# Kernel tuning notes

Measured on AMD Instinct MI355X. Metric: run time of the kernel, lower is better.

The kernel has to match this reference:

```python
import jax, jax.numpy as jnp
import numpy as np

DIM = 256
NUM_HEADS = 8


def setup_inputs() -> dict:
    key = jax.random.key(0)
    ks = jax.random.split(key, 8)
    B, H, W = 2, 64, 64
    s = 0.02
    return {
        "query": jax.random.normal(ks[0], (B, H, W, DIM), jnp.float32),
        "sim": jax.random.normal(ks[1], (B, H, W, DIM), jnp.float32),
        "Wq": jax.random.normal(ks[2], (DIM, DIM), jnp.float32) * s,
        "bq": jnp.zeros((DIM,), jnp.float32),
        "Wkv": jax.random.normal(ks[3], (DIM, 2 * DIM), jnp.float32) * s,
        "bkv": jnp.zeros((2 * DIM,), jnp.float32),
        "Wp": jax.random.normal(ks[4], (DIM, DIM), jnp.float32) * s,
        "bp": jnp.zeros((DIM,), jnp.float32),
    }


def reference(query, sim, Wq, bq, Wkv, bkv, Wp, bp):
    B, H, W, dim = query.shape
    nh = NUM_HEADS
    dh = dim // nh
    scale = dh ** (-0.5)
    S = H * W

    # projections
    q = (query.reshape(B, S, dim) @ Wq + bq).reshape(B, S, nh, dh)
    kv = (sim.reshape(B, S, dim) @ Wkv + bkv).reshape(B, S, 2, nh, dh)
    k = kv[:, :, 0]  # [B,S,nh,dh]
    v = kv[:, :, 1]

    # attention: scores [B,nh,S,S]
    attn = jnp.einsum('bqhd,bkhd->bhqk', q * scale, k)
    attn = jax.nn.softmax(attn, axis=-1)
    x = jnp.einsum('bhqk,bkhd->bqhd', attn, v)  # [B,S,nh,dh]
    x = x.reshape(B, H, W, dim)
    return x @ Wp + bp
```

## Files before the change

### kernel.cpp

```cpp
#include <hip/hip_runtime.h>
#include <hip/hip_bf16.h>
#include <math.h>


#define SCALE 0.17677669529663687f
#define LOG2E 1.4426950408889634f

typedef __attribute__((ext_vector_type(8))) short short8;
typedef __attribute__((ext_vector_type(8))) _Float16 half8;
typedef __attribute__((ext_vector_type(4))) float f32x4;
typedef __attribute__((ext_vector_type(2))) unsigned int uintx2;

static __device__ __forceinline__ float fexp2(float x) {
#if __has_builtin(__builtin_amdgcn_exp2f)
    return __builtin_amdgcn_exp2f(x);
#else
    return exp2f(x);
#endif
}
static __device__ __forceinline__ unsigned int pk_f16(float a, float b) {
    union { _Float16 h[2]; unsigned int u; } x;
    x.h[0] = (_Float16)a; x.h[1] = (_Float16)b;
    return x.u;
}
static __device__ __forceinline__ unsigned short f2h(float x) {
    _Float16 h = (_Float16)x;
    union { _Float16 h; unsigned short s; } u; u.h = h;
    return u.s;
}
static __device__ __forceinline__ float h2f(unsigned short s) {
    union { _Float16 h; unsigned short s; } u; u.s = s;
    return (float)u.h;
}

static __device__ __forceinline__ half8 p_to_frag(unsigned int u0, unsigned int u1,
                                                  unsigned int u2, unsigned int u3) {
    uintx2 a = __builtin_amdgcn_permlane32_swap(u0, u2, false, false);
    uintx2 b = __builtin_amdgcn_permlane32_swap(u1, u3, false, false);
    uintx2 c = __builtin_amdgcn_permlane16_swap(a.x, a.y, false, false);
    uintx2 d = __builtin_amdgcn_permlane16_swap(b.x, b.y, false, false);
    union { unsigned int u[4]; half8 h; } pu;
    pu.u[0] = c.x; pu.u[1] = d.x; pu.u[2] = c.y; pu.u[3] = d.y;
    return pu.h;
}

__global__ __launch_bounds__(256) void prep(
    const float* __restrict__ Wq, const float* __restrict__ Wkv,
    const float* __restrict__ Wp, unsigned short* __restrict__ wfp)
{
    __shared__ float T[64][68];
    const int bb = blockIdx.x, t = threadIdx.x;
    const int mat = bb >> 4, tile = bb & 15;
    const int kr0 = (tile >> 2) * 64;
    const int nc0 = (tile & 3) * 64;
    const float* src; int ldw, cb; float sc = 1.f;
    if (mat == 0)      { src = Wq;  ldw = 256; cb = 0;   sc = SCALE * LOG2E; }
    else if (mat == 1) { src = Wkv; ldw = 512; cb = 0;   }
    else if (mat == 2) { src = Wkv; ldw = 512; cb = 256; }
    else               { src = Wp;  ldw = 256; cb = 0;   }
    {
        const int rl = t >> 4, c4 = (t & 15) * 4;
#pragma unroll
        for (int rr = 0; rr < 4; ++rr) {
            float4 v = *(const float4*)&src[(long long)(kr0 + rr * 16 + rl) * ldw + cb + nc0 + c4];
            T[rr * 16 + rl][c4 + 0] = v.x; T[rr * 16 + rl][c4 + 1] = v.y;
            T[rr * 16 + rl][c4 + 2] = v.z; T[rr * 16 + rl][c4 + 3] = v.w;
        }
    }
    __syncthreads();
    {
        const int nl = t >> 2, kl0 = (t & 3) * 16;
        const long long orow = (long long)(mat * 256 + nc0 + nl) * 256 + kr0 + kl0;
        union { unsigned short s[16]; uint4 u[2]; } ph;
#pragma unroll
        for (int j = 0; j < 16; ++j)
            ph.s[j] = f2h(T[kl0 + j][nl] * sc);
        *(uint4*)&wfp[orow] = ph.u[0];
        *(uint4*)&wfp[orow + 8] = ph.u[1];
    }
}

__global__ __launch_bounds__(256) void gemm_qkv(
    const float* __restrict__ query, const float* __restrict__ sim,
    const unsigned short* __restrict__ wfp,
    const float* __restrict__ bq, const float* __restrict__ bkv,
    unsigned short* __restrict__ qbuf, unsigned short* __restrict__ kbuf,
    unsigned short* __restrict__ vTb)
{
    __shared__ unsigned short Xs[64 * 40], WsA[64 * 40], WsB[64 * 40];

    const int t = threadIdx.x, wave = t >> 6, lane = t & 63;
    const int col = lane & 15, quad = lane >> 4;
    const int by = blockIdx.y;
    const bool isQ = (by < 4);
    const int n0 = (isQ ? by : by - 4) * 64;
    const int m0 = blockIdx.x * 64;
    const float* __restrict__ X = isQ ? query : sim;
    const int wrowA = (isQ ? 0 : 256) + n0;
    const int wrowB = 512 + n0;
    const int srow = t >> 2, spart = (t & 3) * 8;

    const f32x4 zero = {0.f, 0.f, 0.f, 0.f};
    f32x4 accA[4] = {zero, zero, zero, zero};
    f32x4 accV[4] = {zero, zero, zero, zero};

    for (int kt = 0; kt < 8; ++kt) {
        const int k0 = kt * 32;
        const float* xp = &X[(long long)(m0 + srow) * 256 + k0 + spart];
        float4 xa = *(const float4*)xp;
        float4 xb = *(const float4*)(xp + 4);
        float xv[8] = {xa.x, xa.y, xa.z, xa.w, xb.x, xb.y, xb.z, xb.w};
        union { unsigned short s[8]; uint4 u; } ph;
#pragma unroll
        for (int j = 0; j < 8; ++j) ph.s[j] = f2h(xv[j]);
        uint4 wa = *(const uint4*)&wfp[(long long)(wrowA + srow) * 256 + k0 + spart];
        uint4 wb;
        if (!isQ) wb = *(const uint4*)&wfp[(long long)(wrowB + srow) * 256 + k0 + spart];
        __syncthreads();
        *(uint4*)&Xs[srow * 40 + spart] = ph.u;
        *(uint4*)&WsA[srow * 40 + spart] = wa;
        if (!isQ) *(uint4*)&WsB[srow * 40 + spart] = wb;
        __syncthreads();

        half8 aX = *(const half8*)(Xs + (wave * 16 + col) * 40 + quad * 8);
#pragma unroll
        for (int nt = 0; nt < 4; ++nt) {
            half8 b = *(const half8*)(WsA + (nt * 16 + col) * 40 + quad * 8);
            accA[nt] = __builtin_amdgcn_mfma_f32_16x16x32_f16(aX, b, accA[nt], 0, 0, 0);
        }
        if (!isQ) {
            half8 aW = *(const half8*)(WsB + (wave * 16 + col) * 40 + quad * 8);
#pragma unroll
            for (int nt = 0; nt < 4; ++nt) {
                half8 b = *(const half8*)(Xs + (nt * 16 + col) * 40 + quad * 8);
                accV[nt] = __builtin_amdgcn_mfma_f32_16x16x32_f16(aW, b, accV[nt], 0, 0, 0);
            }
        }
    }

    if (isQ) {
#pragma unroll
        for (int nt = 0; nt < 4; ++nt) {
            int n = n0 + nt * 16 + col;
            int h = n >> 5, d = n & 31;
            float bias = bq[n] * (SCALE * LOG2E);
#pragma unroll
            for (int r = 0; r < 4; ++r) {
                int mg = m0 + wave * 16 + quad * 4 + r;
                int b = mg >> 12, sidx = mg & 4095;
                qbuf[((long long)(b * 8 + h) * 4096 + sidx) * 32 + d] = f2h(accA[nt][r] + bias);
            }
        }
    } else {
#pragma unroll
        for (int nt = 0; nt < 4; ++nt) {
            int n = n0 + nt * 16 + col;
            int h = n >> 5, d = n & 31;
            float bias = bkv[n];
#pragma unroll
            for (int r = 0; r < 4; ++r) {
                int mg = m0 + wave * 16 + quad * 4 + r;
                int b = mg >> 12, sidx = mg & 4095;
                kbuf[((long long)(b * 8 + h) * 4096 + sidx) * 32 + d] = f2h(accA[nt][r] + bias);
            }
        }
#pragma unroll
        for (int nt = 0; nt < 4; ++nt) {
            int s = m0 + nt * 16 + col;
            int b = s >> 12, sidx = s & 4095;
#pragma unroll
            for (int r = 0; r < 4; ++r) {
                int dcol = n0 + wave * 16 + quad * 4 + r;
                int h = dcol >> 5, dd = dcol & 31;
                float bias = bkv[256 + dcol];
                vTb[((long long)((b * 8 + h) * 32 + dd)) * 4096 + sidx] = f2h(accV[nt][r] + bias);
            }
        }
    }
}

__global__ __launch_bounds__(256) void flash_mfma(
    const unsigned short* __restrict__ qbuf,
    const unsigned short* __restrict__ kbuf,
    const unsigned short* __restrict__ vT,
    unsigned short* __restrict__ xpart, float* __restrict__ lpart)
{
    __shared__ unsigned short Ks[128 * 40];
    __shared__ unsigned short Vt[32 * 152];

    const int t = threadIdx.x;
    const int wave = t >> 6, lane = t & 63;
    const int col = lane & 15, quad = lane >> 4;
    const int qb = blockIdx.x & 31;
    const int bh = (blockIdx.x >> 5) & 15;
    const int ks = blockIdx.x >> 9;
    const int q0 = qb * 128 + wave * 32;
    const long long kvbase = (long long)bh * 4096 * 32;

    const half8 qf0 = *(const half8*)(qbuf + kvbase + (long long)(q0 + col) * 32 + quad * 8);
    const half8 qf1 = *(const half8*)(qbuf + kvbase + (long long)(q0 + 16 + col) * 32 + quad * 8);

    const f32x4 zero = {0.f, 0.f, 0.f, 0.f};
    f32x4 o00 = zero, o01 = zero, o10 = zero, o11 = zero;
    float l0 = 0.f, l1 = 0.f;

    const int krow = t >> 2, kpart = (t & 3) * 8;
    const int vrow = t >> 4, vpart = (t & 15) * 8;

    for (int kt0 = 0; kt0 < 8; ++kt0) {
        const int kt = ks * 8 + kt0;
        uint4 kg0 = *(const uint4*)(kbuf + kvbase + (long long)(kt * 128 + krow) * 32 + kpart);
        uint4 kg1 = *(const uint4*)(kbuf + kvbase + (long long)(kt * 128 + krow + 64) * 32 + kpart);
        uint4 vg0 = *(const uint4*)(vT + ((long long)(bh * 32 + vrow)) * 4096 + kt * 128 + vpart);
        uint4 vg1 = *(const uint4*)(vT + ((long long)(bh * 32 + vrow + 16)) * 4096 + kt * 128 + vpart);
        __syncthreads();
        *(uint4*)(Ks + krow * 40 + kpart) = kg0;
        *(uint4*)(Ks + (krow + 64) * 40 + kpart) = kg1;
        *(uint4*)(Vt + vrow * 152 + vpart) = vg0;
        *(uint4*)(Vt + (vrow + 16) * 152 + vpart) = vg1;
        __syncthreads();

#pragma unroll
        for (int sb = 0; sb < 4; ++sb) {
            const int kb = sb * 32;
            half8 a0 = *(const half8*)(Ks + (kb + col) * 40 + quad * 8);
            half8 a1 = *(const half8*)(Ks + (kb + 16 + col) * 40 + quad * 8);
            half8 v0 = *(const half8*)(Vt + col * 152 + kb + quad * 8);
            half8 v1 = *(const half8*)(Vt + (16 + col) * 152 + kb + quad * 8);
            {
                f32x4 c0 = __builtin_amdgcn_mfma_f32_16x16x32_f16(a0, qf0, zero, 0, 0, 0);
                f32x4 c1 = __builtin_amdgcn_mfma_f32_16x16x32_f16(a1, qf0, zero, 0, 0, 0);
                float p0 = fexp2(c0[0]), p1 = fexp2(c0[1]), p2 = fexp2(c0[2]), p3 = fexp2(c0[3]);
                float p4 = fexp2(c1[0]), p5 = fexp2(c1[1]), p6 = fexp2(c1[2]), p7 = fexp2(c1[3]);
                l0 += ((p0 + p1) + (p2 + p3)) + ((p4 + p5) + (p6 + p7));
                half8 pf = p_to_frag(pk_f16(p0, p1), pk_f16(p2, p3),
                                     pk_f16(p4, p5), pk_f16(p6, p7));
                o00 = __builtin_amdgcn_mfma_f32_16x16x32_f16(v0, pf, o00, 0, 0, 0);
                o01 = __builtin_amdgcn_mfma_f32_16x16x32_f16(v1, pf, o01, 0, 0, 0);
            }
            {
                f32x4 c0 = __builtin_amdgcn_mfma_f32_16x16x32_f16(a0, qf1, zero, 0, 0, 0);
                f32x4 c1 = __builtin_amdgcn_mfma_f32_16x16x32_f16(a1, qf1, zero, 0, 0, 0);
                float p0 = fexp2(c0[0]), p1 = fexp2(c0[1]), p2 = fexp2(c0[2]), p3 = fexp2(c0[3]);
                float p4 = fexp2(c1[0]), p5 = fexp2(c1[1]), p6 = fexp2(c1[2]), p7 = fexp2(c1[3]);
                l1 += ((p0 + p1) + (p2 + p3)) + ((p4 + p5) + (p6 + p7));
                half8 pf = p_to_frag(pk_f16(p0, p1), pk_f16(p2, p3),
                                     pk_f16(p4, p5), pk_f16(p6, p7));
                o10 = __builtin_amdgcn_mfma_f32_16x16x32_f16(v0, pf, o10, 0, 0, 0);
                o11 = __builtin_amdgcn_mfma_f32_16x16x32_f16(v1, pf, o11, 0, 0, 0);
            }
        }
    }

    l0 += __shfl_xor(l0, 16, 64); l0 += __shfl_xor(l0, 32, 64);
    l1 += __shfl_xor(l1, 16, 64); l1 += __shfl_xor(l1, 32, 64);

    const int b = bh >> 3, hh = bh & 7;
    unsigned short* xp = xpart + (long long)ks * 2097152;
    {
        unsigned short* rp = xp + ((long long)(b * 4096 + q0 + col)) * 256 + hh * 32;
        union { unsigned short s[4]; uint2 u; } pa, pb2;
#pragma unroll
        for (int r = 0; r < 4; ++r) { pa.s[r] = f2h(o00[r]); pb2.s[r] = f2h(o01[r]); }
        *(uint2*)(rp + quad * 4) = pa.u;
        *(uint2*)(rp + 16 + quad * 4) = pb2.u;
    }
    {
        unsigned short* rp = xp + ((long long)(b * 4096 + q0 + 16 + col)) * 256 + hh * 32;
        union { unsigned short s[4]; uint2 u; } pa, pb2;
#pragma unroll
        for (int r = 0; r < 4; ++r) { pa.s[r] = f2h(o10[r]); pb2.s[r] = f2h(o11[r]); }
        *(uint2*)(rp + quad * 4) = pa.u;
        *(uint2*)(rp + 16 + quad * 4) = pb2.u;
    }

    if (quad == 0)      lpart[ks * 65536 + bh * 4096 + q0 + col] = l0;
    else if (quad == 1) lpart[ks * 65536 + bh * 4096 + q0 + 16 + col] = l1;
}

__global__ __launch_bounds__(256) void gemm_outp(
    const unsigned short* __restrict__ xpart, const float* __restrict__ lpart,
    const unsigned short* __restrict__ wfp,
    const float* __restrict__ bp, float* __restrict__ out)
{
    __shared__ unsigned short XsH[64 * 40], XsL[64 * 40], Ws[64 * 40];

    const int t = threadIdx.x, wave = t >> 6, lane = t & 63;
    const int col = lane & 15, quad = lane >> 4;
    const int n0 = blockIdx.y * 64;
    const int m0 = blockIdx.x * 64;
    const int wrow0 = 768 + n0;
    const int srow = t >> 2, spart = (t & 3) * 8;
    const int r = m0 + srow;
    const int bidx = r >> 12, s = r & 4095;

    const f32x4 zero = {0.f, 0.f, 0.f, 0.f};
    f32x4 acc[4] = {zero, zero, zero, zero};

    for (int kt = 0; kt < 8; ++kt) {
        const int k0 = kt * 32;
        float lsum = lpart[(bidx * 8 + kt) * 4096 + s]
                   + lpart[65536 + (bidx * 8 + kt) * 4096 + s]
                   + lpart[131072 + (bidx * 8 + kt) * 4096 + s]
                   + lpart[196608 + (bidx * 8 + kt) * 4096 + s];
        const float linv = 1.f / lsum;

        union { unsigned short s4[8]; uint4 u; } p[4];
#pragma unroll
        for (int ss = 0; ss < 4; ++ss)
            p[ss].u = *(const uint4*)&xpart[(long long)ss * 2097152 +
                                            (long long)r * 256 + k0 + spart];
        union { unsigned short s4[8]; uint4 u; } ph, pl;
#pragma unroll
        for (int j = 0; j < 8; ++j) {
            float xv = (h2f(p[0].s4[j]) + h2f(p[1].s4[j]) +
                        h2f(p[2].s4[j]) + h2f(p[3].s4[j])) * linv;
            unsigned short h = f2h(xv);
            ph.s4[j] = h;
            pl.s4[j] = f2h(xv - h2f(h));
        }
        uint4 wh = *(const uint4*)&wfp[(long long)(wrow0 + srow) * 256 + k0 + spart];
        __syncthreads();
        *(uint4*)&XsH[srow * 40 + spart] = ph.u;
        *(uint4*)&XsL[srow * 40 + spart] = pl.u;
        *(uint4*)&Ws[srow * 40 + spart] = wh;
        __syncthreads();

        half8 a_h = *(const half8*)(XsH + (wave * 16 + col) * 40 + quad * 8);
        half8 a_l = *(const half8*)(XsL + (wave * 16 + col) * 40 + quad * 8);
#pragma unroll
        for (int nt = 0; nt < 4; ++nt) {
            half8 b = *(const half8*)(Ws + (nt * 16 + col) * 40 + quad * 8);
            acc[nt] = __builtin_amdgcn_mfma_f32_16x16x32_f16(a_h, b, acc[nt], 0, 0, 0);
            acc[nt] = __builtin_amdgcn_mfma_f32_16x16x32_f16(a_l, b, acc[nt], 0, 0, 0);
        }
    }

#pragma unroll
    for (int nt = 0; nt < 4; ++nt) {
        int n = n0 + nt * 16 + col;
        float bias = bp[n];
#pragma unroll
        for (int rr = 0; rr < 4; ++rr) {
            int mg = m0 + wave * 16 + quad * 4 + rr;
            out[(long long)mg * 256 + n] = acc[nt][rr] + bias;
        }
    }
}

extern "C" void kernel_launch(void* const* d_in, const int* in_sizes, int n_in,
                              void* d_out, int out_size, void* d_ws, size_t ws_size,
                              hipStream_t stream) {
    const float* query = (const float*)d_in[0];
    const float* sim   = (const float*)d_in[1];
    const float* Wq    = (const float*)d_in[2];
    const float* bq    = (const float*)d_in[3];
    const float* Wkv   = (const float*)d_in[4];
    const float* bkv   = (const float*)d_in[5];
    const float* Wp    = (const float*)d_in[6];
    const float* bp    = (const float*)d_in[7];
    float* out = (float*)d_out;

    unsigned short* wsb = (unsigned short*)d_ws;
    unsigned short* qbuf = wsb;
    unsigned short* kbuf = wsb + 2097152;
    unsigned short* vT   = wsb + 4194304;
    unsigned short* wfp  = wsb + 6291456;
    unsigned short* xpart = wsb + 6553600;
    float* lpart = (float*)(wsb + 14942208);

    prep      <<<dim3(64),     256, 0, stream>>>(Wq, Wkv, Wp, wfp);
    gemm_qkv  <<<dim3(128, 8), 256, 0, stream>>>(query, sim, wfp, bq, bkv,
                                                 qbuf, kbuf, vT);
    flash_mfma<<<dim3(2048),   256, 0, stream>>>(qbuf, kbuf, vT, xpart, lpart);
    gemm_outp <<<dim3(128, 4), 256, 0, stream>>>(xpart, lpart, wfp, bp, out);
}
```

Baseline: 164.4 us.

## Halve KV split count and route P fragments through LDS instead of permlane

The flash kernel now splits the key sequence into 2 chunks of 16 tiles instead of 4 chunks of 8, halving the grid and the partial outputs that the projection kernel must read and sum. The P-to-MFMA-operand conversion switches from permlane32/16 swaps to a per-wave LDS round trip. The split change cuts partial-result traffic and reduction work but lowers parallelism. The LDS path adds shared memory use and store/load latency, with no explicit wave barrier between the write and the read.

```diff
diff --git a/kernel.cpp b/kernel.cpp
--- a/kernel.cpp
+++ b/kernel.cpp
@@ -9,7 +9,6 @@
 typedef __attribute__((ext_vector_type(8))) short short8;
 typedef __attribute__((ext_vector_type(8))) _Float16 half8;
 typedef __attribute__((ext_vector_type(4))) float f32x4;
-typedef __attribute__((ext_vector_type(2))) unsigned int uintx2;
 
 static __device__ __forceinline__ float fexp2(float x) {
 #if __has_builtin(__builtin_amdgcn_exp2f)
@@ -31,17 +30,6 @@
 static __device__ __forceinline__ float h2f(unsigned short s) {
     union { _Float16 h; unsigned short s; } u; u.s = s;
     return (float)u.h;
-}
-
-static __device__ __forceinline__ half8 p_to_frag(unsigned int u0, unsigned int u1,
-                                                  unsigned int u2, unsigned int u3) {
-    uintx2 a = __builtin_amdgcn_permlane32_swap(u0, u2, false, false);
-    uintx2 b = __builtin_amdgcn_permlane32_swap(u1, u3, false, false);
-    uintx2 c = __builtin_amdgcn_permlane16_swap(a.x, a.y, false, false);
-    uintx2 d = __builtin_amdgcn_permlane16_swap(b.x, b.y, false, false);
-    union { unsigned int u[4]; half8 h; } pu;
-    pu.u[0] = c.x; pu.u[1] = d.x; pu.u[2] = c.y; pu.u[3] = d.y;
-    return pu.h;
 }
 
 __global__ __launch_bounds__(256) void prep(
@@ -187,6 +175,7 @@
 {
     __shared__ unsigned short Ks[128 * 40];
     __shared__ unsigned short Vt[32 * 152];
+    __shared__ unsigned short Pb[8][640];
 
     const int t = threadIdx.x;
     const int wave = t >> 6, lane = t & 63;
@@ -196,6 +185,8 @@
     const int ks = blockIdx.x >> 9;
     const int q0 = qb * 128 + wave * 32;
     const long long kvbase = (long long)bh * 4096 * 32;
+    unsigned short* pb0 = Pb[wave * 2];
+    unsigned short* pb1 = Pb[wave * 2 + 1];
 
     const half8 qf0 = *(const half8*)(qbuf + kvbase + (long long)(q0 + col) * 32 + quad * 8);
     const half8 qf1 = *(const half8*)(qbuf + kvbase + (long long)(q0 + 16 + col) * 32 + quad * 8);
@@ -207,8 +198,8 @@
     const int krow = t >> 2, kpart = (t & 3) * 8;
     const int vrow = t >> 4, vpart = (t & 15) * 8;
 
-    for (int kt0 = 0; kt0 < 8; ++kt0) {
-        const int kt = ks * 8 + kt0;
+    for (int kt0 = 0; kt0 < 16; ++kt0) {
+        const int kt = ks * 16 + kt0;
         uint4 kg0 = *(const uint4*)(kbuf + kvbase + (long long)(kt * 128 + krow) * 32 + kpart);
         uint4 kg1 = *(const uint4*)(kbuf + kvbase + (long long)(kt * 128 + krow + 64) * 32 + kpart);
         uint4 vg0 = *(const uint4*)(vT + ((long long)(bh * 32 + vrow)) * 4096 + kt * 128 + vpart);
@@ -233,8 +224,11 @@
                 float p0 = fexp2(c0[0]), p1 = fexp2(c0[1]), p2 = fexp2(c0[2]), p3 = fexp2(c0[3]);
                 float p4 = fexp2(c1[0]), p5 = fexp2(c1[1]), p6 = fexp2(c1[2]), p7 = fexp2(c1[3]);
                 l0 += ((p0 + p1) + (p2 + p3)) + ((p4 + p5) + (p6 + p7));
-                half8 pf = p_to_frag(pk_f16(p0, p1), pk_f16(p2, p3),
-                                     pk_f16(p4, p5), pk_f16(p6, p7));
+                uint2 w0 = make_uint2(pk_f16(p0, p1), pk_f16(p2, p3));
+                uint2 w1 = make_uint2(pk_f16(p4, p5), pk_f16(p6, p7));
+                *(uint2*)(pb0 + col * 40 + quad * 4) = w0;
+                *(uint2*)(pb0 + col * 40 + 16 + quad * 4) = w1;
+                half8 pf = *(const half8*)(pb0 + col * 40 + quad * 8);
                 o00 = __builtin_amdgcn_mfma_f32_16x16x32_f16(v0, pf, o00, 0, 0, 0);
                 o01 = __builtin_amdgcn_mfma_f32_16x16x32_f16(v1, pf, o01, 0, 0, 0);
             }
@@ -244,8 +238,11 @@
                 float p0 = fexp2(c0[0]), p1 = fexp2(c0[1]), p2 = fexp2(c0[2]), p3 = fexp2(c0[3]);
                 float p4 = fexp2(c1[0]), p5 = fexp2(c1[1]), p6 = fexp2(c1[2]), p7 = fexp2(c1[3]);
                 l1 += ((p0 + p1) + (p2 + p3)) + ((p4 + p5) + (p6 + p7));
-                half8 pf = p_to_frag(pk_f16(p0, p1), pk_f16(p2, p3),
-                                     pk_f16(p4, p5), pk_f16(p6, p7));
+                uint2 w0 = make_uint2(pk_f16(p0, p1), pk_f16(p2, p3));
+                uint2 w1 = make_uint2(pk_f16(p4, p5), pk_f16(p6, p7));
+                *(uint2*)(pb1 + col * 40 + quad * 4) = w0;
+                *(uint2*)(pb1 + col * 40 + 16 + quad * 4) = w1;
+                half8 pf = *(const half8*)(pb1 + col * 40 + quad * 8);
                 o10 = __builtin_amdgcn_mfma_f32_16x16x32_f16(v0, pf, o10, 0, 0, 0);
                 o11 = __builtin_amdgcn_mfma_f32_16x16x32_f16(v1, pf, o11, 0, 0, 0);
             }
@@ -300,21 +297,18 @@
     for (int kt = 0; kt < 8; ++kt) {
         const int k0 = kt * 32;
         float lsum = lpart[(bidx * 8 + kt) * 4096 + s]
-                   + lpart[65536 + (bidx * 8 + kt) * 4096 + s]
-                   + lpart[131072 + (bidx * 8 + kt) * 4096 + s]
-                   + lpart[196608 + (bidx * 8 + kt) * 4096 + s];
+                   + lpart[65536 + (bidx * 8 + kt) * 4096 + s];
         const float linv = 1.f / lsum;
 
-        union { unsigned short s4[8]; uint4 u; } p[4];
-#pragma unroll
-        for (int ss = 0; ss < 4; ++ss)
+        union { unsigned short s4[8]; uint4 u; } p[2];
+#pragma unroll
+        for (int ss = 0; ss < 2; ++ss)
             p[ss].u = *(const uint4*)&xpart[(long long)ss * 2097152 +
                                             (long long)r * 256 + k0 + spart];
         union { unsigned short s4[8]; uint4 u; } ph, pl;
 #pragma unroll
         for (int j = 0; j < 8; ++j) {
-            float xv = (h2f(p[0].s4[j]) + h2f(p[1].s4[j]) +
-                        h2f(p[2].s4[j]) + h2f(p[3].s4[j])) * linv;
+            float xv = (h2f(p[0].s4[j]) + h2f(p[1].s4[j])) * linv;
             unsigned short h = f2h(xv);
             ph.s4[j] = h;
             pl.s4[j] = f2h(xv - h2f(h));
@@ -372,6 +366,6 @@
     prep      <<<dim3(64),     256, 0, stream>>>(Wq, Wkv, Wp, wfp);
     gemm_qkv  <<<dim3(128, 8), 256, 0, stream>>>(query, sim, wfp, bq, bkv,
                                                  qbuf, kbuf, vT);
-    flash_mfma<<<dim3(2048),   256, 0, stream>>>(qbuf, kbuf, vT, xpart, lpart);
+    flash_mfma<<<dim3(1024),   256, 0, stream>>>(qbuf, kbuf, vT, xpart, lpart);
     gemm_outp <<<dim3(128, 4), 256, 0, stream>>>(xpart, lpart, wfp, bp, out);
 }
```

Result: faster. 159.3 us (-3.1%).
